# Kernel optimization log

Measured on AMD Instinct MI355X. Metric: run time of the kernel, lower is better.

## Reference

```python
import jax, jax.numpy as jnp
import numpy as np

IN_CHANNELS = 192
KERNEL_SIZE = 3
GROUPS = 1
N_ITER = 3  # power_it_niter


def _gram_conv(K):
    """Gram step of the conv operator: G[a, b] = sum_o corr(K[o, a], K[o, b]).

    K: (co, ci, k, k) -> (ci, ci, 2k-1, 2k-1). This is the kernel of M^T M
    where M is the (zero-padded) conv operator with kernel K.
    """
    k = K.shape[-1]
    lhs = jnp.transpose(K, (1, 0, 2, 3))  # batch = a-index, channels = o
    rhs = jnp.transpose(K, (1, 0, 2, 3))  # out-chan = b-index, in-chan = o
    return jax.lax.conv_general_dilated(
        lhs, rhs, window_strides=(1, 1),
        padding=[(k - 1, k - 1), (k - 1, k - 1)],
        dimension_numbers=("NCHW", "OIHW", "NCHW"))


def _sigma_one_group(K, n_iter):
    """Gram-iteration spectral-norm estimate (Delattre et al. 2024).

    sigma(K_0) ~= prod_t f_t^(1/2^t) * ||K_T||_F^(1/2^T), f_t = Frobenius norm
    before each Gram squaring (normalization keeps values in fp range).
    """
    log_sigma = jnp.asarray(0.0, K.dtype)
    for t in range(n_iter):  # static unroll: kernel spatial size grows k -> 2k-1
        f = jnp.sqrt(jnp.sum(K * K))
        K = K / f
        log_sigma = log_sigma + jnp.log(f) / (2.0 ** t)
        K = _gram_conv(K)
    f_final = jnp.sqrt(jnp.sum(K * K))
    log_sigma = log_sigma + jnp.log(f_final) / (2.0 ** n_iter)
    return jnp.exp(log_sigma)


def compute_delattre2024(K, n_iter):
    # K: (groups, c, c, k, k) -> (groups,) per-group spectral norm estimates
    return jax.vmap(lambda g: _sigma_one_group(g, n_iter))(K)


def setup_inputs() -> dict:
    key = jax.random.key(0)
    kernel = jax.random.normal(
        key, (IN_CHANNELS * GROUPS, IN_CHANNELS, KERNEL_SIZE, KERNEL_SIZE),
        dtype=jnp.float32)
    return {"kernel": kernel}


def reference(kernel):
    g = GROUPS
    c = IN_CHANNELS // GROUPS
    K = kernel.reshape(g, c, c, KERNEL_SIZE, KERNEL_SIZE)
    sigmas = compute_delattre2024(K, N_ITER)  # (groups,)
    K = K / sigmas.reshape(-1, 1, 1, 1, 1)
    return K.reshape(IN_CHANNELS * GROUPS, IN_CHANNELS, KERNEL_SIZE, KERNEL_SIZE)
```

## Files before the change

### kernel.cpp

```cpp
#include <hip/hip_runtime.h>
#include <hip/hip_bf16.h>

typedef __bf16 bf16;
typedef __attribute__((ext_vector_type(8))) __bf16 bf16x8;
typedef __attribute__((ext_vector_type(4))) float f32x4;
typedef __attribute__((ext_vector_type(4))) int i32x4;

#define CH 192
#define MAT (CH * CH)
#define NF 145
#define FSTRIDE (2 * MAT)
#define NELEM (CH * CH * 9)
#define XSCALE 9.765625e-4f
#define W17 0.36959913571644626f


__device__ __forceinline__ int swz8(int c, int r) {
    return (c & ~7) | ((c & 7) ^ (r & 7));
}

__global__ void k_dft(const float* __restrict__ K, bf16* __restrict__ X,
                      float* __restrict__ s3) {
    __shared__ float twc[17], tws[17];
    int bid = blockIdx.x;
    int xcd = bid & 7;
    int r = bid >> 3;
    int g = r / 18, chunk = r % 18;
    int t = threadIdx.x;
    if (bid == 0 && t == 0) *s3 = 0.0f;
    if (t < 17) {
        float s, c;
        __sincosf(-W17 * (float)t, &s, &c);
        twc[t] = c; tws[t] = s;
    }
    int p0 = chunk * 2048 + t * 8;
    int a = p0 / CH, o0 = p0 % CH;
    float kv[8][9];
#pragma unroll
    for (int j = 0; j < 8; ++j) {
        const float* src = K + ((size_t)(o0 + j) * CH + a) * 9;
#pragma unroll
        for (int i = 0; i < 9; ++i) kv[j][i] = src[i];
    }
    int sc = swz8(o0 >> 3, a);
    size_t sbase = (size_t)a * CH + sc * 8;
    __syncthreads();
#pragma unroll
    for (int u = 0; u < 5; ++u) {
        int f = xcd + 8 * (g * 5 + u);
        if (f >= NF) continue;
        int fy, fx;
        if (f < 9) { fy = 0; fx = f; }
        else { int uu = f - 9; fy = 1 + uu / 17; fx = uu % 17; }
        float pyr = twc[fy], pyi = tws[fy];
        float pxr = twc[fx], pxi = tws[fx];
        int fx2 = 2 * fx; if (fx2 >= 17) fx2 -= 17;
        int fy2 = 2 * fy; if (fy2 >= 17) fy2 -= 17;
        float px2r = twc[fx2], px2i = tws[fx2];
        float py2r = twc[fy2], py2i = tws[fy2];
        bf16x8 vr, vi;
#pragma unroll
        for (int j = 0; j < 8; ++j) {
            float s0r = kv[j][0] + kv[j][1] * pxr + kv[j][2] * px2r, s0i = kv[j][1] * pxi + kv[j][2] * px2i;
            float s1r = kv[j][3] + kv[j][4] * pxr + kv[j][5] * px2r, s1i = kv[j][4] * pxi + kv[j][5] * px2i;
            float s2r = kv[j][6] + kv[j][7] * pxr + kv[j][8] * px2r, s2i = kv[j][7] * pxi + kv[j][8] * px2i;
            float ar = s0r + pyr * s1r - pyi * s1i + py2r * s2r - py2i * s2i;
            float ai = s0i + pyr * s1i + pyi * s1r + py2r * s2i + py2i * s2r;
            vr[j] = (bf16)(ar * XSCALE);
            vi[j] = (bf16)(ai * XSCALE);
        }
        size_t base = (size_t)f * FSTRIDE + sbase;
        *(i32x4*)(X + base)       = __builtin_bit_cast(i32x4, vr);
        *(i32x4*)(X + base + MAT) = __builtin_bit_cast(i32x4, vi);
    }
}

__global__ __launch_bounds__(1024, 4)
__attribute__((amdgpu_waves_per_eu(4, 4)))
void k_g3(const bf16* __restrict__ X, float* __restrict__ s3) {
    __shared__ __align__(16) bf16 lds[2 * MAT];
    __shared__ float red[16];
    int f = blockIdx.x;
    const bf16* Xf = X + (size_t)f * FSTRIDE;
    int tid = threadIdx.x;
    int lane = tid & 63, w = tid >> 6;
    int ml = lane & 15, kqc = lane >> 4;
    int rb = (w >> 2) * 48;
    int cb = (w & 3) * 48;

    {
        const char* gs = (const char*)Xf;
        char* lb = (char*)lds;
#pragma unroll
        for (int j = 0; j < 9; ++j) {
            __builtin_amdgcn_global_load_lds(
                (const __attribute__((address_space(1))) void*)(gs + (j * 1024 + tid) * 16),
                (__attribute__((address_space(3))) void*)(lb + (j * 1024 + (tid & ~63)) * 16),
                16, 0, 0);
        }
        asm volatile("s_waitcnt vmcnt(0)" ::: "memory");
    }
    __syncthreads();

    int arow[3], abit[3], brow[3], bbit[3];
#pragma unroll
    for (int i = 0; i < 3; ++i) {
        int ra = rb + i * 16 + ml;
        arow[i] = ra * CH; abit[i] = ra & 7;
        int rc = cb + i * 16 + ml;
        brow[i] = rc * CH; bbit[i] = rc & 7;
    }

    f32x4 cr[3][3], ci[3][3];
#pragma unroll 1
    for (int round = 0; round < 3; ++round) {
#pragma unroll
        for (int i = 0; i < 3; ++i)
#pragma unroll
            for (int j = 0; j < 3; ++j) {
                cr[i][j] = f32x4{0.f, 0.f, 0.f, 0.f};
                ci[i][j] = f32x4{0.f, 0.f, 0.f, 0.f};
            }
#pragma unroll
        for (int ks8 = 0; ks8 < 24; ks8 += 4) {
            int c0 = ks8 + kqc;
            bf16x8 ar[3], ai[3];
#pragma unroll
            for (int mt = 0; mt < 3; ++mt) {
                int e = arow[mt] + swz8(c0, abit[mt]) * 8;
                ar[mt] = *(const bf16x8*)&lds[e];
                ai[mt] = *(const bf16x8*)&lds[MAT + e];
            }
#pragma unroll
            for (int nt = 0; nt < 3; ++nt) {
                int e = brow[nt] + swz8(c0, bbit[nt]) * 8;
                bf16x8 br = *(const bf16x8*)&lds[e];
                bf16x8 bi = *(const bf16x8*)&lds[MAT + e];
                i32x4 u = __builtin_bit_cast(i32x4, br);
                u ^= 0x80008000;
                bf16x8 nbr = __builtin_bit_cast(bf16x8, u);
#pragma unroll
                for (int mt = 0; mt < 3; ++mt) {
                    cr[mt][nt] = __builtin_amdgcn_mfma_f32_16x16x32_bf16(ar[mt], br,  cr[mt][nt], 0, 0, 0);
                    cr[mt][nt] = __builtin_amdgcn_mfma_f32_16x16x32_bf16(ai[mt], bi,  cr[mt][nt], 0, 0, 0);
                    ci[mt][nt] = __builtin_amdgcn_mfma_f32_16x16x32_bf16(ar[mt], bi,  ci[mt][nt], 0, 0, 0);
                    ci[mt][nt] = __builtin_amdgcn_mfma_f32_16x16x32_bf16(ai[mt], nbr, ci[mt][nt], 0, 0, 0);
                }
            }
        }
        if (round < 2) {
            __syncthreads();
            int lr = kqc * 4;
#pragma unroll
            for (int mt = 0; mt < 3; ++mt)
#pragma unroll
                for (int nt = 0; nt < 3; ++nt)
#pragma unroll
                    for (int rr = 0; rr < 4; ++rr) {
                        int row = rb + mt * 16 + lr + rr;
                        int col = cb + nt * 16 + ml;
                        int e = row * CH + swz8(col >> 3, row) * 8 + (col & 7);
                        lds[e]       = (bf16)cr[mt][nt][rr];
                        lds[MAT + e] = (bf16)ci[mt][nt][rr];
                    }
            __syncthreads();
        }
    }

    float loc = 0.f;
#pragma unroll
    for (int mt = 0; mt < 3; ++mt)
#pragma unroll
        for (int nt = 0; nt < 3; ++nt)
#pragma unroll
            for (int rr = 0; rr < 4; ++rr)
                loc += cr[mt][nt][rr] * cr[mt][nt][rr] + ci[mt][nt][rr] * ci[mt][nt][rr];
#pragma unroll
    for (int off = 32; off > 0; off >>= 1) loc += __shfl_down(loc, off, 64);
    if (lane == 0) red[w] = loc;
    __syncthreads();
    if (tid == 0) {
        float base = (f == 0) ? 1.0f : 2.0f;
        float acc = 0.f;
#pragma unroll
        for (int i = 0; i < 16; ++i) acc += red[i];
        atomicAdd(s3, base * acc);
    }
}

__global__ void k_scale(const float* __restrict__ K, float* __restrict__ out,
                        const float* __restrict__ s3) {
    float sig = 1024.0f * exp2f(log2f((*s3) * (1.0f / 289.0f)) * 0.0625f);
    float inv = 1.0f / sig;
    int i = (blockIdx.x * 256 + threadIdx.x) * 4;
    f32x4 v = *(const f32x4*)(K + i);
    v *= inv;
    *(f32x4*)(out + i) = v;
}

extern "C" void kernel_launch(void* const* d_in, const int* in_sizes, int n_in,
                              void* d_out, int out_size, void* d_ws, size_t ws_size,
                              hipStream_t stream) {
    const float* K = (const float*)d_in[0];
    float* out = (float*)d_out;
    char* ws = (char*)d_ws;
    float* s3 = (float*)ws;
    bf16* bufX = (bf16*)(ws + 256);

    k_dft<<<8 * 4 * 18, 256, 0, stream>>>(K, bufX, s3);
    k_g3<<<NF, 1024, 0, stream>>>(bufX, s3);
    k_scale<<<NELEM / 1024, 256, 0, stream>>>(K, out, s3);
}
```

Measured before the change: 111.4 us.

## Fuse per-frequency DFT into Gram kernel, replacing spectral buffer with transposed kernel

The separate DFT kernel that wrote 145 bf16 complex spectra to global memory is removed. A small transpose kernel now writes K as (a,o,9) floats, and each Gram block computes its own frequency's DFT directly into LDS from the transposed kernel. This avoids writing and re-reading the large spectral buffer. In exchange, each of the 145 blocks re-reads the whole 1.3MB transposed kernel, mostly from L2, and does the DFT arithmetic inline before its MFMA rounds. MFMA issue order is also interleaved so consecutive instructions do not share an accumulator.

```diff
diff --git a/kernel.cpp b/kernel.cpp
--- a/kernel.cpp
+++ b/kernel.cpp
@@ -9,7 +9,6 @@
 #define CH 192
 #define MAT (CH * CH)
 #define NF 145
-#define FSTRIDE (2 * MAT)
 #define NELEM (CH * CH * 9)
 #define XSCALE 9.765625e-4f
 #define W17 0.36959913571644626f
@@ -19,86 +18,77 @@
     return (c & ~7) | ((c & 7) ^ (r & 7));
 }
 
-__global__ void k_dft(const float* __restrict__ K, bf16* __restrict__ X,
-                      float* __restrict__ s3) {
-    __shared__ float twc[17], tws[17];
-    int bid = blockIdx.x;
-    int xcd = bid & 7;
-    int r = bid >> 3;
-    int g = r / 18, chunk = r % 18;
-    int t = threadIdx.x;
-    if (bid == 0 && t == 0) *s3 = 0.0f;
-    if (t < 17) {
-        float s, c;
-        __sincosf(-W17 * (float)t, &s, &c);
-        twc[t] = c; tws[t] = s;
-    }
-    int p0 = chunk * 2048 + t * 8;
-    int a = p0 / CH, o0 = p0 % CH;
-    float kv[8][9];
-#pragma unroll
-    for (int j = 0; j < 8; ++j) {
-        const float* src = K + ((size_t)(o0 + j) * CH + a) * 9;
-#pragma unroll
-        for (int i = 0; i < 9; ++i) kv[j][i] = src[i];
-    }
-    int sc = swz8(o0 >> 3, a);
-    size_t sbase = (size_t)a * CH + sc * 8;
-    __syncthreads();
-#pragma unroll
-    for (int u = 0; u < 5; ++u) {
-        int f = xcd + 8 * (g * 5 + u);
-        if (f >= NF) continue;
-        int fy, fx;
-        if (f < 9) { fy = 0; fx = f; }
-        else { int uu = f - 9; fy = 1 + uu / 17; fx = uu % 17; }
-        float pyr = twc[fy], pyi = tws[fy];
-        float pxr = twc[fx], pxi = tws[fx];
-        int fx2 = 2 * fx; if (fx2 >= 17) fx2 -= 17;
-        int fy2 = 2 * fy; if (fy2 >= 17) fy2 -= 17;
-        float px2r = twc[fx2], px2i = tws[fx2];
-        float py2r = twc[fy2], py2i = tws[fy2];
-        bf16x8 vr, vi;
-#pragma unroll
-        for (int j = 0; j < 8; ++j) {
-            float s0r = kv[j][0] + kv[j][1] * pxr + kv[j][2] * px2r, s0i = kv[j][1] * pxi + kv[j][2] * px2i;
-            float s1r = kv[j][3] + kv[j][4] * pxr + kv[j][5] * px2r, s1i = kv[j][4] * pxi + kv[j][5] * px2i;
-            float s2r = kv[j][6] + kv[j][7] * pxr + kv[j][8] * px2r, s2i = kv[j][7] * pxi + kv[j][8] * px2i;
-            float ar = s0r + pyr * s1r - pyi * s1i + py2r * s2r - py2i * s2i;
-            float ai = s0i + pyr * s1i + pyi * s1r + py2r * s2i + py2i * s2r;
-            vr[j] = (bf16)(ar * XSCALE);
-            vi[j] = (bf16)(ai * XSCALE);
-        }
-        size_t base = (size_t)f * FSTRIDE + sbase;
-        *(i32x4*)(X + base)       = __builtin_bit_cast(i32x4, vr);
-        *(i32x4*)(X + base + MAT) = __builtin_bit_cast(i32x4, vi);
-    }
-}
+__global__ void k_tr(const float* __restrict__ K, float* __restrict__ Kt,
+                     float* __restrict__ s3) {
+    int p = blockIdx.x * 256 + threadIdx.x;
+    if (p == 0) *s3 = 0.0f;
+    int a = p / CH, o = p % CH;
+    const float* src = K + ((size_t)o * CH + a) * 9;
+    float* dst = Kt + (size_t)p * 9;
+#pragma unroll
+    for (int i = 0; i < 9; ++i) dst[i] = src[i];
+}
+
+#define KVE(j, i) kv4[((j) * 9 + (i)) >> 2][((j) * 9 + (i)) & 3]
 
 __global__ __launch_bounds__(1024, 4)
 __attribute__((amdgpu_waves_per_eu(4, 4)))
-void k_g3(const bf16* __restrict__ X, float* __restrict__ s3) {
+void k_g3(const float* __restrict__ Kt, float* __restrict__ s3) {
     __shared__ __align__(16) bf16 lds[2 * MAT];
+    __shared__ float twc[17], tws[17];
     __shared__ float red[16];
     int f = blockIdx.x;
-    const bf16* Xf = X + (size_t)f * FSTRIDE;
     int tid = threadIdx.x;
     int lane = tid & 63, w = tid >> 6;
     int ml = lane & 15, kqc = lane >> 4;
     int rb = (w >> 2) * 48;
     int cb = (w & 3) * 48;
 
-    {
-        const char* gs = (const char*)Xf;
-        char* lb = (char*)lds;
-#pragma unroll
-        for (int j = 0; j < 9; ++j) {
-            __builtin_amdgcn_global_load_lds(
-                (const __attribute__((address_space(1))) void*)(gs + (j * 1024 + tid) * 16),
-                (__attribute__((address_space(3))) void*)(lb + (j * 1024 + (tid & ~63)) * 16),
-                16, 0, 0);
+    if (tid < 17) {
+        float s, c;
+        __sincosf(-W17 * (float)tid, &s, &c);
+        twc[tid] = c; tws[tid] = s;
+    }
+    __syncthreads();
+
+    int fy, fx;
+    if (f < 9) { fy = 0; fx = f; }
+    else { int uu = f - 9; fy = 1 + uu / 17; fx = uu % 17; }
+    float pyr = twc[fy], pyi = tws[fy];
+    float pxr = twc[fx], pxi = tws[fx];
+    int fx2 = 2 * fx; if (fx2 >= 17) fx2 -= 17;
+    int fy2 = 2 * fy; if (fy2 >= 17) fy2 -= 17;
+    float px2r = twc[fx2], px2i = tws[fx2];
+    float py2r = twc[fy2], py2i = tws[fy2];
+
+#pragma unroll
+    for (int j5 = 0; j5 < 5; ++j5) {
+        int cidx = j5 * 1024 + tid;
+        if (cidx < 4608) {
+            int a = cidx / 24, c = cidx % 24;
+            int o0 = c * 8;
+            const float* src = Kt + ((size_t)a * CH + o0) * 9;
+            f32x4 kv4[18];
+#pragma unroll
+            for (int i = 0; i < 18; ++i) kv4[i] = *(const f32x4*)(src + i * 4);
+            bf16x8 vr, vi;
+#pragma unroll
+            for (int j = 0; j < 8; ++j) {
+                float s0r = KVE(j,0) + KVE(j,1) * pxr + KVE(j,2) * px2r;
+                float s0i = KVE(j,1) * pxi + KVE(j,2) * px2i;
+                float s1r = KVE(j,3) + KVE(j,4) * pxr + KVE(j,5) * px2r;
+                float s1i = KVE(j,4) * pxi + KVE(j,5) * px2i;
+                float s2r = KVE(j,6) + KVE(j,7) * pxr + KVE(j,8) * px2r;
+                float s2i = KVE(j,7) * pxi + KVE(j,8) * px2i;
+                float ar = s0r + pyr * s1r - pyi * s1i + py2r * s2r - py2i * s2i;
+                float ai = s0i + pyr * s1i + pyi * s1r + py2r * s2i + py2i * s2r;
+                vr[j] = (bf16)(ar * XSCALE);
+                vi[j] = (bf16)(ai * XSCALE);
+            }
+            int e = a * CH + swz8(c, a) * 8;
+            *(i32x4*)&lds[e]       = __builtin_bit_cast(i32x4, vr);
+            *(i32x4*)&lds[MAT + e] = __builtin_bit_cast(i32x4, vi);
         }
-        asm volatile("s_waitcnt vmcnt(0)" ::: "memory");
     }
     __syncthreads();
 
@@ -142,8 +132,8 @@
 #pragma unroll
                 for (int mt = 0; mt < 3; ++mt) {
                     cr[mt][nt] = __builtin_amdgcn_mfma_f32_16x16x32_bf16(ar[mt], br,  cr[mt][nt], 0, 0, 0);
+                    ci[mt][nt] = __builtin_amdgcn_mfma_f32_16x16x32_bf16(ar[mt], bi,  ci[mt][nt], 0, 0, 0);
                     cr[mt][nt] = __builtin_amdgcn_mfma_f32_16x16x32_bf16(ai[mt], bi,  cr[mt][nt], 0, 0, 0);
-                    ci[mt][nt] = __builtin_amdgcn_mfma_f32_16x16x32_bf16(ar[mt], bi,  ci[mt][nt], 0, 0, 0);
                     ci[mt][nt] = __builtin_amdgcn_mfma_f32_16x16x32_bf16(ai[mt], nbr, ci[mt][nt], 0, 0, 0);
                 }
             }
@@ -205,9 +195,9 @@
     float* out = (float*)d_out;
     char* ws = (char*)d_ws;
     float* s3 = (float*)ws;
-    bf16* bufX = (bf16*)(ws + 256);
-
-    k_dft<<<8 * 4 * 18, 256, 0, stream>>>(K, bufX, s3);
-    k_g3<<<NF, 1024, 0, stream>>>(bufX, s3);
+    float* Kt = (float*)(ws + 256);
+
+    k_tr<<<NELEM / (256 * 9), 256, 0, stream>>>(K, Kt, s3);
+    k_g3<<<NF, 1024, 0, stream>>>(Kt, s3);
     k_scale<<<NELEM / 1024, 256, 0, stream>>>(K, out, s3);
 }
```

After: 124.4 us. +11.6%, slower.
